# Optimization experiments

Hardware: AMD Instinct MI355X
Metric: run time of the kernel (lower is better)

The kernel has to match this reference:

```python
import jax, jax.numpy as jnp
import numpy as np
import math

S, E, H, D, B, L = 16384, 1152, 16, 72, 16, 1024  # total tokens, embed, heads, head_dim, n_seqs, seq_len


def rotate_half(x):
    x1, x2 = jnp.split(x, 2, axis=-1)
    return jnp.concatenate((-x2, x1), axis=-1)


def setup_inputs() -> dict:
    key = jax.random.key(0)
    ks = jax.random.split(key, 8)
    hidden_states = jax.random.normal(ks[0], (S, E), jnp.float32)
    cu_seqlens = jnp.arange(B + 1, dtype=jnp.int32) * L  # equal-length segments (required by original reshape)
    ang = jax.random.uniform(ks[1], (S, D), jnp.float32, 0.0, 2.0 * math.pi)
    cos, sin = jnp.cos(ang), jnp.sin(ang)
    w = lambda k: jax.random.normal(k, (E, E), jnp.float32) * 0.02
    return {
        'hidden_states': hidden_states,
        'cu_seqlens': cu_seqlens,
        'cos': cos, 'sin': sin,
        'Wq': w(ks[2]), 'bq': jnp.zeros((E,), jnp.float32),
        'Wk': w(ks[3]), 'bk': jnp.zeros((E,), jnp.float32),
        'Wv': w(ks[4]), 'bv': jnp.zeros((E,), jnp.float32),
        'Wo': w(ks[5]), 'bo': jnp.zeros((E,), jnp.float32),
    }


def reference(hidden_states, cu_seqlens, cos, sin, Wq, bq, Wk, bk, Wv, bv, Wo, bo):
    seq_len, embed = hidden_states.shape
    q = (hidden_states @ Wq + bq).reshape(seq_len, H, D)
    k = (hidden_states @ Wk + bk).reshape(seq_len, H, D)
    v = (hidden_states @ Wv + bv).reshape(seq_len, H, D)
    # RoPE, broadcast over heads: cos/sin (S, 1, D)
    c = cos[:, None, :]
    s = sin[:, None, :]
    q = q * c + rotate_half(q) * s
    k = k * c + rotate_half(k) * s
    # varlen -> batched (equal-length segments; padding/mask is a no-op in this regime)
    nb = cu_seqlens.shape[0] - 1
    ls = seq_len // nb
    qb = q.reshape(nb, ls, H, D).transpose(0, 2, 1, 3)  # (B, H, L, D)
    kb = k.reshape(nb, ls, H, D).transpose(0, 2, 1, 3)
    vb = v.reshape(nb, ls, H, D).transpose(0, 2, 1, 3)
    scale = D ** -0.5
    scores = jnp.einsum('bhqd,bhkd->bhqk', qb, kb) * scale
    attn = jax.nn.softmax(scores, axis=-1)
    out = jnp.einsum('bhqk,bhkd->bhqd', attn, vb)
    out = out.transpose(0, 2, 1, 3).reshape(seq_len, embed)
    return out @ Wo + bo
```

## Files before the change

### kernel.cpp

```cpp
#include <hip/hip_runtime.h>

typedef __attribute__((ext_vector_type(8))) short bf16x8;
typedef __attribute__((ext_vector_type(4))) float f32x4;

#define S_LEN 16384
#define EMB   1152
#define NQKV  3456
#define NH    16
#define HD    72

__device__ __forceinline__ unsigned short f2b(float f){
  union { float f; unsigned u; } x; x.f = f;
  unsigned r = x.u + 0x7fffu + ((x.u >> 16) & 1u);
  return (unsigned short)(r >> 16);
}
__device__ __forceinline__ float b2f(unsigned short h){
  union { unsigned u; float f; } x; x.u = ((unsigned)h) << 16; return x.f;
}
__device__ __forceinline__ void glds16(const void* g, void* l){
  __builtin_amdgcn_global_load_lds((const __attribute__((address_space(1))) void*)g,
                                   (__attribute__((address_space(3))) void*)l, 16, 0, 0);
}

__global__ void prep_hs(const float* __restrict__ hs, unsigned short* __restrict__ hsb){
  long i = (long)blockIdx.x*256 + threadIdx.x;
  const long n8 = (long)S_LEN*EMB/8;
  if (i >= n8) return;
  const float4* p = (const float4*)(hs + i*8);
  float4 a = p[0], b = p[1];
  uint4 o;
  o.x = f2b(a.x) | ((unsigned)f2b(a.y)<<16);
  o.y = f2b(a.z) | ((unsigned)f2b(a.w)<<16);
  o.z = f2b(b.x) | ((unsigned)f2b(b.y)<<16);
  o.w = f2b(b.z) | ((unsigned)f2b(b.w)<<16);
  *(uint4*)(hsb + i*8) = o;
}

__global__ void prep_w(const float* __restrict__ Wq, const float* __restrict__ Wk,
                       const float* __restrict__ Wv, const float* __restrict__ Wo,
                       const float* __restrict__ bq, const float* __restrict__ bk,
                       const float* __restrict__ bv,
                       unsigned short* __restrict__ wqkv, unsigned short* __restrict__ wot,
                       float* __restrict__ biasq){
  long i = (long)blockIdx.x*256 + threadIdx.x;
  if (i < NQKV)
    biasq[i] = (i < 1152) ? bq[i] : (i < 2304 ? bk[i-1152] : bv[i-2304]);
  if (i >= (long)4608*1152) return;
  int k  = (int)(i % 1152);
  int n  = (int)(i / 1152);
  int sel = n / 1152, nn = n % 1152;
  const float* W = (sel==0)?Wq:(sel==1)?Wk:(sel==2)?Wv:Wo;
  unsigned short v = f2b(W[(long)k*1152 + nn]);
  if (sel < 3) wqkv[(long)n*1152 + k] = v;
  else         wot [(long)nn*1152 + k] = v;
}

template<int OUTF32>
__global__ __launch_bounds__(512, 2) void gemm8(
    const unsigned short* __restrict__ A,
    const unsigned short* __restrict__ Bt,
    const float* __restrict__ bias,
    unsigned short* __restrict__ Cb,
    float* __restrict__ Cf,
    int N, int K, int NXT)
{
  __shared__ unsigned short lds[3*24576];
  const int BUFE = 24576;
  int tid = threadIdx.x, lane = tid & 63, wave = tid >> 6;
  int wm = wave >> 1, wn = wave & 1;
  int lr = lane & 15, hi = lane >> 4, rx = lr & 7;

  int nblk = gridDim.x, bid = blockIdx.x;
  int cpx = nblk >> 3;
  int swz = (bid & 7)*cpx + (bid >> 3);
  long ar0 = (long)(swz / NXT) * 256;
  long bc0 = (long)(swz % NXT) * 128;

  const unsigned short* srcp[6];
  int dsto[6];
  #pragma unroll
  for (int i=0;i<6;i++){
    int f = i*512 + tid;
    dsto[i] = f*8;
    if (i < 4){
      int row = f >> 3, cL = f & 7;
      srcp[i] = A + (ar0 + row)*(long)K + (cL ^ (row & 7))*8;
    } else {
      int fb = f - 2048;
      int row = fb >> 3, cL = fb & 7;
      srcp[i] = Bt + (bc0 + row)*(long)K + (cL ^ (row & 7))*8;
    }
  }

  int aoff[4][2], boff[4][2];
  #pragma unroll
  for (int mi=0;mi<4;mi++)
    #pragma unroll
    for (int ks=0;ks<2;ks++)
      aoff[mi][ks] = (wm*64 + mi*16 + lr)*64 + (((ks*4 + hi) ^ rx)*8);
  #pragma unroll
  for (int ni=0;ni<4;ni++)
    #pragma unroll
    for (int ks=0;ks<2;ks++)
      boff[ni][ks] = 16384 + (wn*64 + ni*16 + lr)*64 + (((ks*4 + hi) ^ rx)*8);

  f32x4 acc[4][4];
  #pragma unroll
  for (int mi=0;mi<4;mi++)
    #pragma unroll
    for (int ni=0;ni<4;ni++) acc[mi][ni] = (f32x4){0.f,0.f,0.f,0.f};

  const int nT = K >> 6;
  auto STG = [&](int T){
    unsigned short* lb_ = lds + (T % 3)*BUFE;
    long k0_ = (long)T * 64;
    #pragma unroll
    for (int i=0;i<6;i++) glds16(srcp[i] + k0_, lb_ + dsto[i]);
  };

  STG(0); STG(1);
  asm volatile("s_waitcnt vmcnt(6)" ::: "memory");
  __builtin_amdgcn_s_barrier();

  for (int t=0; t<nT; ++t){
    if (t+2 < nT) STG(t+2);
    const unsigned short* lb = lds + (t % 3)*BUFE;
    #pragma unroll
    for (int ks=0;ks<2;ks++){
      bf16x8 af[4], bfv[4];
      #pragma unroll
      for (int mi=0;mi<4;mi++) af[mi]  = *(const bf16x8*)(lb + aoff[mi][ks]);
      #pragma unroll
      for (int ni=0;ni<4;ni++) bfv[ni] = *(const bf16x8*)(lb + boff[ni][ks]);
      #pragma unroll
      for (int mi=0;mi<4;mi++)
        #pragma unroll
        for (int ni=0;ni<4;ni++)
          acc[mi][ni] = __builtin_amdgcn_mfma_f32_16x16x32_bf16(af[mi], bfv[ni], acc[mi][ni], 0,0,0);
    }
    if (t+1 < nT){
      if (t+2 < nT) asm volatile("s_waitcnt vmcnt(6)" ::: "memory");
      else          asm volatile("s_waitcnt vmcnt(0)" ::: "memory");
      __builtin_amdgcn_s_barrier();
    }
  }

  int orow = hi*4, ocol = lr;
  #pragma unroll
  for (int mi=0;mi<4;mi++){
    long r0 = ar0 + wm*64 + mi*16 + orow;
    #pragma unroll
    for (int ni=0;ni<4;ni++){
      long c = bc0 + wn*64 + ni*16 + ocol;
      float bb = bias[c];
      #pragma unroll
      for (int r=0;r<4;r++){
        float v = acc[mi][ni][r] + bb;
        if (OUTF32) Cf[(r0+r)*(long)N + c] = v;
        else        Cb[(r0+r)*(long)N + c] = f2b(v);
      }
    }
  }
}

__global__ void rope_k(unsigned short* __restrict__ qkv,
                       const float* __restrict__ cs, const float* __restrict__ sn){
  long i = (long)blockIdx.x*256 + threadIdx.x;
  const long tot = 2L*S_LEN*NH*36;
  if (i >= tot) return;
  int d = (int)(i % 36); long t2 = i/36;
  int h = (int)(t2 % NH); long t3 = t2/NH;
  int s = (int)(t3 % S_LEN); int qk = (int)(t3 / S_LEN);
  long base = (long)s*NQKV + (long)qk*1152 + h*HD;
  float x1 = b2f(qkv[base + d]), x2 = b2f(qkv[base + d + 36]);
  float c1 = cs[(long)s*HD + d], c2 = cs[(long)s*HD + d + 36];
  float s1 = sn[(long)s*HD + d], s2 = sn[(long)s*HD + d + 36];
  qkv[base + d]      = f2b(x1*c1 - x2*s1);
  qkv[base + d + 36] = f2b(x2*c2 + x1*s2);
}

__global__ void transpose_v(const unsigned short* __restrict__ qkv, unsigned short* __restrict__ vt){
  __shared__ unsigned short t[64*72];
  int tid = threadIdx.x;
  int kt = blockIdx.x, bh = blockIdx.y;
  int b = bh >> 4, h = bh & 15;
  const unsigned short* src = qkv + ((long)b*1024 + (long)kt*64)*NQKV + 2304 + h*HD;
  #pragma unroll
  for (int i=0;i<3;i++){
    int idx = i*256 + tid;
    if (idx < 576){
      int r = idx/9, c = (idx%9)*8;
      *(uint4*)&t[r*72 + c] = *(const uint4*)&src[(long)r*NQKV + c];
    }
  }
  __syncthreads();
  unsigned short* dst = vt + (long)bh*HD*1024 + (long)kt*64;
  #pragma unroll
  for (int i=0;i<3;i++){
    int idx = i*256 + tid;
    if (idx < 576){
      int d = idx>>3, k8 = (idx&7)*8;
      unsigned short v[8];
      #pragma unroll
      for (int j=0;j<8;j++) v[j] = t[(k8+j)*72 + d];
      uint4 o;
      o.x = v[0] | ((unsigned)v[1]<<16);
      o.y = v[2] | ((unsigned)v[3]<<16);
      o.z = v[4] | ((unsigned)v[5]<<16);
      o.w = v[6] | ((unsigned)v[7]<<16);
      *(uint4*)&dst[(long)d*1024 + k8] = o;
    }
  }
}

__global__ __launch_bounds__(512, 1) void attn3_k(
    const unsigned short* __restrict__ qkv,
    const unsigned short* __restrict__ vt,
    unsigned short* __restrict__ aout)
{
  __shared__ unsigned short Ks[64*72 + 32];
  __shared__ unsigned short Vts[80*72];
  __shared__ unsigned short Pt[8][16*72];
  int tid = threadIdx.x, lane = tid & 63, w = tid >> 6;
  int G = lane >> 4, l15 = lane & 15;
  int bid = blockIdx.x;
  int wg = (bid & 7)*256 + (bid >> 3);
  int bh = wg >> 3, qt = wg & 7;
  int b = bh >> 4, h = bh & 15;

  const unsigned short* kgbase = qkv + ((long)b*1024)*NQKV + 1152 + h*HD;
  const unsigned short* vgbase = vt + (long)bh*HD*1024;

  int key0 = tid/9,        kc0 = (tid%9)*8;
  bool ex  = (tid < 64);
  int ki1  = 512 + tid;
  int key1 = ki1/9,        kc1 = (ki1%9)*8;
  long koff0 = (long)key0*NQKV + kc0;  int kdst0 = key0*72 + kc0;
  long koff1 = (long)key1*NQKV + kc1;  int kdst1 = key1*72 + kc1;
  int vd0 = tid>>3,        vc0 = (tid&7)*8;
  int vi1 = 512 + tid;
  int vd1 = vi1>>3,        vc1 = (vi1&7)*8;
  long voff0 = (long)vd0*1024 + vc0;   int vdst0 = vd0*72 + vc0;
  long voff1 = (long)vd1*1024 + vc1;   int vdst1 = vd1*72 + vc1;

  uint4 pf0, pf1, pf2, pf3;
  #define STAGE_ISSUE(KT) do { \
    const unsigned short* kg_ = kgbase + (long)(KT)*64*NQKV; \
    const unsigned short* vg_ = vgbase + (KT)*64; \
    pf0 = *(const uint4*)(kg_ + koff0); \
    pf2 = *(const uint4*)(vg_ + voff0); \
    if (ex){ pf1 = *(const uint4*)(kg_ + koff1); pf3 = *(const uint4*)(vg_ + voff1); } \
  } while(0)
  #define STAGE_WRITE() do { \
    *(uint4*)&Ks[kdst0]  = pf0; \
    *(uint4*)&Vts[vdst0] = pf2; \
    if (ex){ *(uint4*)&Ks[kdst1] = pf1; *(uint4*)&Vts[vdst1] = pf3; } \
  } while(0)

  const uint4 z4 = make_uint4(0,0,0,0);
  if (tid < 4)  *(uint4*)&Ks[64*72 + tid*8] = z4;
  if (tid < 72) *(uint4*)&Vts[72*72 + tid*8] = z4;

  long sq0 = (long)b*1024 + qt*128 + w*16;
  const unsigned short* qrow = qkv + (sq0 + l15)*NQKV + h*HD;
  bf16x8 qf[3];
  #pragma unroll
  for (int ds=0; ds<3; ds++){
    int d0 = ds*32 + 8*G;
    if (d0 <= 64) qf[ds] = *(const bf16x8*)(qrow + d0);
    else          qf[ds] = (bf16x8){0,0,0,0,0,0,0,0};
  }

  f32x4 oacc[5];
  #pragma unroll
  for (int nd=0; nd<5; nd++) oacc[nd] = (f32x4){0.f,0.f,0.f,0.f};
  float m = -1e30f, lsum = 0.f;
  const float SL = 0.11785113f * 1.44269504f;

  STAGE_ISSUE(0);
  STAGE_WRITE();
  __syncthreads();

  unsigned short* pw = Pt[w];

  for (int kt=0; kt<16; kt++){
    if (kt < 15) STAGE_ISSUE(kt+1);

    f32x4 sacc[4];
    #pragma unroll
    for (int ni=0; ni<4; ni++) sacc[ni] = (f32x4){0.f,0.f,0.f,0.f};
    #pragma unroll
    for (int ds=0; ds<3; ds++){
      #pragma unroll
      for (int ni=0; ni<4; ni++){
        bf16x8 kf = *(const bf16x8*)&Ks[(ni*16 + l15)*72 + ds*32 + 8*G];
        sacc[ni] = __builtin_amdgcn_mfma_f32_16x16x32_bf16(kf, qf[ds], sacc[ni], 0,0,0);
      }
    }

    float tm = -1e30f;
    #pragma unroll
    for (int ni=0; ni<4; ni++)
      #pragma unroll
      for (int r=0; r<4; r++) tm = fmaxf(tm, sacc[ni][r]);
    tm = fmaxf(tm, __shfl_xor(tm, 16));
    tm = fmaxf(tm, __shfl_xor(tm, 32));
    float mn = fmaxf(m, tm);
    float corr = __builtin_amdgcn_exp2f((m - mn)*SL);
    m = mn; lsum *= corr;
    float msl = m * SL;
    float rs = 0.f;
    #pragma unroll
    for (int ni=0; ni<4; ni++)
      #pragma unroll
      for (int r=0; r<4; r++){
        float p = __builtin_amdgcn_exp2f(__builtin_fmaf(sacc[ni][r], SL, -msl));
        sacc[ni][r] = p; rs += p;
      }
    rs += __shfl_xor(rs, 16);
    rs += __shfl_xor(rs, 32);
    lsum += rs;

    #pragma unroll
    for (int ni=0; ni<4; ni++){
      unsigned u0 = (unsigned)f2b(sacc[ni][0]) | ((unsigned)f2b(sacc[ni][1])<<16);
      unsigned u1 = (unsigned)f2b(sacc[ni][2]) | ((unsigned)f2b(sacc[ni][3])<<16);
      *(unsigned*)&pw[l15*72 + ni*16 + 4*G]     = u0;
      *(unsigned*)&pw[l15*72 + ni*16 + 4*G + 2] = u1;
    }

    float c0 = __shfl(corr, 4*G + 0);
    float c1 = __shfl(corr, 4*G + 1);
    float c2 = __shfl(corr, 4*G + 2);
    float c3 = __shfl(corr, 4*G + 3);
    #pragma unroll
    for (int nd=0; nd<5; nd++){
      oacc[nd][0] *= c0; oacc[nd][1] *= c1; oacc[nd][2] *= c2; oacc[nd][3] *= c3;
    }

    #pragma unroll
    for (int ks=0; ks<2; ks++){
      bf16x8 pA = *(const bf16x8*)&pw[l15*72 + ks*32 + 8*G];
      #pragma unroll
      for (int nd=0; nd<5; nd++){
        bf16x8 vf = *(const bf16x8*)&Vts[(nd*16 + l15)*72 + ks*32 + 8*G];
        oacc[nd] = __builtin_amdgcn_mfma_f32_16x16x32_bf16(pA, vf, oacc[nd], 0,0,0);
      }
    }

    if (kt < 15){
      __syncthreads();
      STAGE_WRITE();
      __syncthreads();
    }
  }

  float inv = 1.f / lsum;
  float i0 = __shfl(inv, 4*G + 0);
  float i1 = __shfl(inv, 4*G + 1);
  float i2 = __shfl(inv, 4*G + 2);
  float i3 = __shfl(inv, 4*G + 3);
  #pragma unroll
  for (int nd=0; nd<5; nd++){
    int d = nd*16 + l15;
    if (d < HD){
      long base = (sq0 + 4*G)*EMB + h*HD + d;
      aout[base        ] = f2b(oacc[nd][0]*i0);
      aout[base +   EMB] = f2b(oacc[nd][1]*i1);
      aout[base + 2*EMB] = f2b(oacc[nd][2]*i2);
      aout[base + 3*EMB] = f2b(oacc[nd][3]*i3);
    }
  }
  #undef STAGE_ISSUE
  #undef STAGE_WRITE
}

extern "C" void kernel_launch(void* const* d_in, const int* in_sizes, int n_in,
                              void* d_out, int out_size, void* d_ws, size_t ws_size,
                              hipStream_t stream){
  const float* hs = (const float*)d_in[0];
  const float* cs = (const float*)d_in[2];
  const float* sn = (const float*)d_in[3];
  const float* Wq = (const float*)d_in[4];
  const float* bq = (const float*)d_in[5];
  const float* Wk = (const float*)d_in[6];
  const float* bk = (const float*)d_in[7];
  const float* Wv = (const float*)d_in[8];
  const float* bv = (const float*)d_in[9];
  const float* Wo = (const float*)d_in[10];
  const float* bo = (const float*)d_in[11];
  float* out = (float*)d_out;

  char* ws = (char*)d_ws;
  size_t off = 0;
  unsigned short* hsb  = (unsigned short*)(ws + off); off += (size_t)S_LEN*EMB*2;
  unsigned short* wqkv = (unsigned short*)(ws + off); off += (size_t)NQKV*EMB*2;
  unsigned short* wot  = (unsigned short*)(ws + off); off += (size_t)EMB*EMB*2;
  float*          biasq= (float*)(ws + off);          off += (size_t)NQKV*4 + 2560;
  unsigned short* qkv  = (unsigned short*)(ws + off); off += (size_t)S_LEN*NQKV*2;
  unsigned short* vt   = (unsigned short*)(ws + off); off += (size_t)256*HD*1024*2;

  prep_hs<<<(S_LEN*EMB/8 + 255)/256, 256, 0, stream>>>(hs, hsb);
  prep_w<<<((long)4608*1152 + 255)/256, 256, 0, stream>>>(Wq, Wk, Wv, Wo, bq, bk, bv, wqkv, wot, biasq);
  gemm8<0><<<dim3((NQKV/128)*(S_LEN/256)), 512, 0, stream>>>(hsb, wqkv, biasq, qkv, nullptr, NQKV, EMB, NQKV/128);
  rope_k<<<(2L*S_LEN*NH*36 + 255)/256, 256, 0, stream>>>(qkv, cs, sn);
  transpose_v<<<dim3(16, 256), 256, 0, stream>>>(qkv, vt);
  attn3_k<<<2048, 512, 0, stream>>>(qkv, vt, hsb);
  gemm8<1><<<dim3((EMB/128)*(S_LEN/256)), 512, 0, stream>>>(hsb, wot, bo, nullptr, out, EMB, EMB, EMB/128);
}
```

Baseline: 614.2 us.

## Tile weight transpose, double-buffer attention K/V, skip unchanged rescale

Weight conversion now uses a 64x64 LDS-tiled transpose, so both the reads and the writes are coalesced, and the bias packing moves into prep_hs. The attention kernel double-buffers K and V tiles in LDS, which removes one __syncthreads per iteration. It also skips the output rescale when no row max grew anywhere in the wave, and packs P to bf16 with a hardware instruction. The costs are more LDS per block, a wave-uniform branch, and round-to-nearest conversion that may differ slightly from the software rounding it replaces.

```diff
diff --git a/kernel.cpp b/kernel.cpp
--- a/kernel.cpp
+++ b/kernel.cpp
@@ -21,9 +21,18 @@
   __builtin_amdgcn_global_load_lds((const __attribute__((address_space(1))) void*)g,
                                    (__attribute__((address_space(3))) void*)l, 16, 0, 0);
 }
-
-__global__ void prep_hs(const float* __restrict__ hs, unsigned short* __restrict__ hsb){
+__device__ __forceinline__ unsigned cvt_pk_bf16(float lo, float hi){
+  unsigned r;
+  asm("v_cvt_pk_bf16_f32 %0, %1, %2" : "=v"(r) : "v"(lo), "v"(hi));
+  return r;
+}
+
+__global__ void prep_hs(const float* __restrict__ hs, unsigned short* __restrict__ hsb,
+                        const float* __restrict__ bq, const float* __restrict__ bk,
+                        const float* __restrict__ bv, float* __restrict__ biasq){
   long i = (long)blockIdx.x*256 + threadIdx.x;
+  if (i < NQKV)
+    biasq[i] = (i < 1152) ? bq[i] : (i < 2304 ? bk[i-1152] : bv[i-2304]);
   const long n8 = (long)S_LEN*EMB/8;
   if (i >= n8) return;
   const float4* p = (const float4*)(hs + i*8);
@@ -36,23 +45,31 @@
   *(uint4*)(hsb + i*8) = o;
 }
 
-__global__ void prep_w(const float* __restrict__ Wq, const float* __restrict__ Wk,
-                       const float* __restrict__ Wv, const float* __restrict__ Wo,
-                       const float* __restrict__ bq, const float* __restrict__ bk,
-                       const float* __restrict__ bv,
-                       unsigned short* __restrict__ wqkv, unsigned short* __restrict__ wot,
-                       float* __restrict__ biasq){
-  long i = (long)blockIdx.x*256 + threadIdx.x;
-  if (i < NQKV)
-    biasq[i] = (i < 1152) ? bq[i] : (i < 2304 ? bk[i-1152] : bv[i-2304]);
-  if (i >= (long)4608*1152) return;
-  int k  = (int)(i % 1152);
-  int n  = (int)(i / 1152);
-  int sel = n / 1152, nn = n % 1152;
-  const float* W = (sel==0)?Wq:(sel==1)?Wk:(sel==2)?Wv:Wo;
-  unsigned short v = f2b(W[(long)k*1152 + nn]);
-  if (sel < 3) wqkv[(long)n*1152 + k] = v;
-  else         wot [(long)nn*1152 + k] = v;
+__global__ __launch_bounds__(256) void prep_wt(
+    const float* __restrict__ Wq, const float* __restrict__ Wk,
+    const float* __restrict__ Wv, const float* __restrict__ Wo,
+    unsigned short* __restrict__ wqkv, unsigned short* __restrict__ wot){
+  __shared__ unsigned short t[64][70];
+  int mz = blockIdx.z;
+  const float* W = (mz==0)?Wq:(mz==1)?Wk:(mz==2)?Wv:Wo;
+  unsigned short* dst = (mz<3) ? (wqkv + (size_t)mz*1152*1152) : wot;
+  int k0 = blockIdx.y*64, n0 = blockIdx.x*64;
+  int tid = threadIdx.x;
+  int r = tid>>4, c4 = (tid&15)*4;
+  #pragma unroll
+  for (int i=0;i<4;i++){
+    int rr = r + i*16;
+    float4 v = *(const float4*)&W[(size_t)(k0+rr)*1152 + n0 + c4];
+    t[rr][c4+0]=f2b(v.x); t[rr][c4+1]=f2b(v.y); t[rr][c4+2]=f2b(v.z); t[rr][c4+3]=f2b(v.w);
+  }
+  __syncthreads();
+  #pragma unroll
+  for (int i=0;i<4;i++){
+    int nn = r + i*16;
+    unsigned short o0 = t[c4+0][nn], o1 = t[c4+1][nn], o2 = t[c4+2][nn], o3 = t[c4+3][nn];
+    uint2 o; o.x = o0 | ((unsigned)o1<<16); o.y = o2 | ((unsigned)o3<<16);
+    *(uint2*)&dst[(size_t)(n0+nn)*1152 + k0 + c4] = o;
+  }
 }
 
 template<int OUTF32>
@@ -213,13 +230,13 @@
   }
 }
 
-__global__ __launch_bounds__(512, 1) void attn3_k(
+__global__ __launch_bounds__(512, 1) void attn4_k(
     const unsigned short* __restrict__ qkv,
     const unsigned short* __restrict__ vt,
     unsigned short* __restrict__ aout)
 {
-  __shared__ unsigned short Ks[64*72 + 32];
-  __shared__ unsigned short Vts[80*72];
+  __shared__ unsigned short Ks[2][64*72 + 32];
+  __shared__ unsigned short Vts[2][80*72];
   __shared__ unsigned short Pt[8][16*72];
   int tid = threadIdx.x, lane = tid & 63, w = tid >> 6;
   int G = lane >> 4, l15 = lane & 15;
@@ -251,15 +268,15 @@
     pf2 = *(const uint4*)(vg_ + voff0); \
     if (ex){ pf1 = *(const uint4*)(kg_ + koff1); pf3 = *(const uint4*)(vg_ + voff1); } \
   } while(0)
-  #define STAGE_WRITE() do { \
-    *(uint4*)&Ks[kdst0]  = pf0; \
-    *(uint4*)&Vts[vdst0] = pf2; \
-    if (ex){ *(uint4*)&Ks[kdst1] = pf1; *(uint4*)&Vts[vdst1] = pf3; } \
+  #define STAGE_WRITE(BUF) do { \
+    *(uint4*)&Ks[BUF][kdst0]  = pf0; \
+    *(uint4*)&Vts[BUF][vdst0] = pf2; \
+    if (ex){ *(uint4*)&Ks[BUF][kdst1] = pf1; *(uint4*)&Vts[BUF][vdst1] = pf3; } \
   } while(0)
 
   const uint4 z4 = make_uint4(0,0,0,0);
-  if (tid < 4)  *(uint4*)&Ks[64*72 + tid*8] = z4;
-  if (tid < 72) *(uint4*)&Vts[72*72 + tid*8] = z4;
+  if (tid < 4){ *(uint4*)&Ks[0][64*72 + tid*8] = z4; *(uint4*)&Ks[1][64*72 + tid*8] = z4; }
+  if (tid < 72){ *(uint4*)&Vts[0][72*72 + tid*8] = z4; *(uint4*)&Vts[1][72*72 + tid*8] = z4; }
 
   long sq0 = (long)b*1024 + qt*128 + w*16;
   const unsigned short* qrow = qkv + (sq0 + l15)*NQKV + h*HD;
@@ -278,13 +295,15 @@
   const float SL = 0.11785113f * 1.44269504f;
 
   STAGE_ISSUE(0);
-  STAGE_WRITE();
+  STAGE_WRITE(0);
   __syncthreads();
 
   unsigned short* pw = Pt[w];
 
   for (int kt=0; kt<16; kt++){
     if (kt < 15) STAGE_ISSUE(kt+1);
+    const unsigned short* ksb = Ks[kt & 1];
+    const unsigned short* vsb = Vts[kt & 1];
 
     f32x4 sacc[4];
     #pragma unroll
@@ -293,7 +312,7 @@
     for (int ds=0; ds<3; ds++){
       #pragma unroll
       for (int ni=0; ni<4; ni++){
-        bf16x8 kf = *(const bf16x8*)&Ks[(ni*16 + l15)*72 + ds*32 + 8*G];
+        bf16x8 kf = *(const bf16x8*)&ksb[(ni*16 + l15)*72 + ds*32 + 8*G];
         sacc[ni] = __builtin_amdgcn_mfma_f32_16x16x32_bf16(kf, qf[ds], sacc[ni], 0,0,0);
       }
     }
@@ -305,9 +324,13 @@
       for (int r=0; r<4; r++) tm = fmaxf(tm, sacc[ni][r]);
     tm = fmaxf(tm, __shfl_xor(tm, 16));
     tm = fmaxf(tm, __shfl_xor(tm, 32));
-    float mn = fmaxf(m, tm);
-    float corr = __builtin_amdgcn_exp2f((m - mn)*SL);
-    m = mn; lsum *= corr;
+    bool grow = __any(tm > m);
+    float corr = 1.f;
+    if (grow){
+      float mn = fmaxf(m, tm);
+      corr = __builtin_amdgcn_exp2f((m - mn)*SL);
+      m = mn; lsum *= corr;
+    }
     float msl = m * SL;
     float rs = 0.f;
     #pragma unroll
@@ -323,19 +346,21 @@
 
     #pragma unroll
     for (int ni=0; ni<4; ni++){
-      unsigned u0 = (unsigned)f2b(sacc[ni][0]) | ((unsigned)f2b(sacc[ni][1])<<16);
-      unsigned u1 = (unsigned)f2b(sacc[ni][2]) | ((unsigned)f2b(sacc[ni][3])<<16);
-      *(unsigned*)&pw[l15*72 + ni*16 + 4*G]     = u0;
-      *(unsigned*)&pw[l15*72 + ni*16 + 4*G + 2] = u1;
-    }
-
-    float c0 = __shfl(corr, 4*G + 0);
-    float c1 = __shfl(corr, 4*G + 1);
-    float c2 = __shfl(corr, 4*G + 2);
-    float c3 = __shfl(corr, 4*G + 3);
-    #pragma unroll
-    for (int nd=0; nd<5; nd++){
-      oacc[nd][0] *= c0; oacc[nd][1] *= c1; oacc[nd][2] *= c2; oacc[nd][3] *= c3;
+      uint2 o;
+      o.x = cvt_pk_bf16(sacc[ni][0], sacc[ni][1]);
+      o.y = cvt_pk_bf16(sacc[ni][2], sacc[ni][3]);
+      *(uint2*)&pw[l15*72 + ni*16 + 4*G] = o;
+    }
+
+    if (grow){
+      float c0 = __shfl(corr, 4*G + 0);
+      float c1 = __shfl(corr, 4*G + 1);
+      float c2 = __shfl(corr, 4*G + 2);
+      float c3 = __shfl(corr, 4*G + 3);
+      #pragma unroll
+      for (int nd=0; nd<5; nd++){
+        oacc[nd][0] *= c0; oacc[nd][1] *= c1; oacc[nd][2] *= c2; oacc[nd][3] *= c3;
+      }
     }
 
     #pragma unroll
@@ -343,14 +368,13 @@
       bf16x8 pA = *(const bf16x8*)&pw[l15*72 + ks*32 + 8*G];
       #pragma unroll
       for (int nd=0; nd<5; nd++){
-        bf16x8 vf = *(const bf16x8*)&Vts[(nd*16 + l15)*72 + ks*32 + 8*G];
+        bf16x8 vf = *(const bf16x8*)&vsb[(nd*16 + l15)*72 + ks*32 + 8*G];
         oacc[nd] = __builtin_amdgcn_mfma_f32_16x16x32_bf16(pA, vf, oacc[nd], 0,0,0);
       }
     }
 
     if (kt < 15){
-      __syncthreads();
-      STAGE_WRITE();
+      STAGE_WRITE((kt+1) & 1);
       __syncthreads();
     }
   }
@@ -400,11 +424,11 @@
   unsigned short* qkv  = (unsigned short*)(ws + off); off += (size_t)S_LEN*NQKV*2;
   unsigned short* vt   = (unsigned short*)(ws + off); off += (size_t)256*HD*1024*2;
 
-  prep_hs<<<(S_LEN*EMB/8 + 255)/256, 256, 0, stream>>>(hs, hsb);
-  prep_w<<<((long)4608*1152 + 255)/256, 256, 0, stream>>>(Wq, Wk, Wv, Wo, bq, bk, bv, wqkv, wot, biasq);
+  prep_hs<<<(S_LEN*EMB/8 + 255)/256, 256, 0, stream>>>(hs, hsb, bq, bk, bv, biasq);
+  prep_wt<<<dim3(18, 18, 4), 256, 0, stream>>>(Wq, Wk, Wv, Wo, wqkv, wot);
   gemm8<0><<<dim3((NQKV/128)*(S_LEN/256)), 512, 0, stream>>>(hsb, wqkv, biasq, qkv, nullptr, NQKV, EMB, NQKV/128);
   rope_k<<<(2L*S_LEN*NH*36 + 255)/256, 256, 0, stream>>>(qkv, cs, sn);
   transpose_v<<<dim3(16, 256), 256, 0, stream>>>(qkv, vt);
-  attn3_k<<<2048, 512, 0, stream>>>(qkv, vt, hsb);
+  attn4_k<<<2048, 512, 0, stream>>>(qkv, vt, hsb);
   gemm8<1><<<dim3((EMB/128)*(S_LEN/256)), 512, 0, stream>>>(hsb, wot, bo, nullptr, out, EMB, EMB, EMB/128);
 }
```

After: 619.6 us. No clear change (+0.9%).
